# Kernel tuning notes

Hardware: AMD Instinct MI355X
Metric: run time of the kernel (lower is better)

Reference implementation:

```python
import jax, jax.numpy as jnp
import numpy as np

B, CIN, CCTX, K, V, T, KS = 8, 512, 512, 64, 256, 1024, 23
EPS = 1e-5


def _bn(z, gamma, beta):
    # train-mode BatchNorm1d over (batch, time) per channel, biased variance
    mean = jnp.mean(z, axis=(0, 2), keepdims=True)
    var = jnp.mean((z - mean) ** 2, axis=(0, 2), keepdims=True)
    return (z - mean) * jax.lax.rsqrt(var + EPS) * gamma[None, :, None] + beta[None, :, None]


def setup_inputs() -> dict:
    key = jax.random.key(0)
    ks = jax.random.split(key, 10)
    x = jax.random.normal(ks[0], (B, CIN, T), dtype=jnp.float32)
    context = jax.random.normal(ks[1], (B, CCTX, T), dtype=jnp.float32)
    Wq = jax.random.normal(ks[2], (K, CIN), dtype=jnp.float32) * (CIN ** -0.5)
    bq = jnp.zeros((K,), dtype=jnp.float32)
    Wk = jax.random.normal(ks[3], (K, CCTX), dtype=jnp.float32) * (CCTX ** -0.5)
    bk = jnp.zeros((K,), dtype=jnp.float32)
    Wv = jax.random.normal(ks[4], (V, CCTX), dtype=jnp.float32) * (CCTX ** -0.5)
    bv = jnp.zeros((V,), dtype=jnp.float32)
    gamma_q = jnp.ones((K,), dtype=jnp.float32)
    beta_q = jnp.zeros((K,), dtype=jnp.float32)
    gamma_v = jnp.ones((V,), dtype=jnp.float32)
    beta_v = jnp.zeros((V,), dtype=jnp.float32)
    pos_w = jax.random.normal(ks[5], (K, KS), dtype=jnp.float32) * (KS ** -0.5)
    pos_b = jnp.zeros((K,), dtype=jnp.float32)
    return {"x": x, "context": context, "Wq": Wq, "bq": bq, "Wk": Wk, "bk": bk,
            "Wv": Wv, "bv": bv, "gamma_q": gamma_q, "beta_q": beta_q,
            "gamma_v": gamma_v, "beta_v": beta_v, "pos_w": pos_w, "pos_b": pos_b}


def reference(x, context, Wq, bq, Wk, bk, Wv, bv,
              gamma_q, beta_q, gamma_v, beta_v, pos_w, pos_b):
    # 1x1 conv1d == channel matmul
    queries = jnp.einsum('bct,kc->bkt', x, Wq) + bq[None, :, None]          # (B,K,T)
    keys = jnp.einsum('bct,kc->bkt', context, Wk) + bk[None, :, None]       # (B,K,T)
    values = jnp.einsum('bct,vc->bvt', context, Wv) + bv[None, :, None]     # (B,V,T)

    norm_keys = jax.nn.softmax(keys, axis=-1)                               # softmax over T
    queries = _bn(queries, gamma_q, beta_q)
    values = _bn(values, gamma_v, beta_v)

    q_t = jnp.transpose(queries, (0, 2, 1))                                 # (B,T,K)
    v_t = jnp.transpose(values, (0, 2, 1))                                  # (B,T,V)

    content_lambda = jnp.einsum('bkt,btv->bkv', norm_keys, v_t)             # (B,K,V)

    # positional conv2d: kernel (K,1,KS,1), padding (KS//2, 0) along T
    lhs = v_t[:, None, :, :]                                                # (B,1,T,V)
    rhs = pos_w[:, None, :, None]                                           # (K,1,KS,1)
    pl = jax.lax.conv_general_dilated(
        lhs, rhs, window_strides=(1, 1),
        padding=[(KS // 2, KS // 2), (0, 0)],
        dimension_numbers=('NCHW', 'OIHW', 'NCHW'))
    pl = pl + pos_b[None, :, None, None]                                    # (B,K,T,V)
    pl = jnp.transpose(pl, (0, 2, 1, 3))                                    # (B,T,K,V)

    content_out = jnp.einsum('btk,bkv->btv', q_t, content_lambda)           # (B,T,V)
    positional_out = jnp.einsum('btk,btkv->btv', q_t, pl)                   # (B,T,V)

    return jnp.transpose(content_out + positional_out, (0, 2, 1))           # (B,V,T)
```

## Files before the change

kernel.cpp:

```cpp
#include <hip/hip_runtime.h>
#include <math.h>

#define B_ 8
#define CIN_ 512
#define K_ 64
#define V_ 256
#define T_ 1024
#define KS_ 23
#define EPS_ 1e-5f
#define NTC_ 8

typedef __attribute__((ext_vector_type(8))) short bf16x8;
typedef __attribute__((ext_vector_type(4))) float f32x4;

__device__ __forceinline__ unsigned short f2bf(float f) {
    union { float f; unsigned u; } x; x.f = f;
    unsigned r = x.u + 0x7fffu + ((x.u >> 16) & 1u);
    return (unsigned short)(r >> 16);
}
__device__ __forceinline__ float bf2f(unsigned short h) {
    union { unsigned u; float f; } x; x.u = ((unsigned)h) << 16;
    return x.f;
}

__device__ __forceinline__ void gload16(const unsigned short* g, unsigned short* l) {
    __builtin_amdgcn_global_load_lds(
        (const __attribute__((address_space(1))) unsigned int*)(const void*)g,
        (__attribute__((address_space(3))) unsigned int*)(void*)l, 16, 0, 0);
}

__global__ __launch_bounds__(256) void prep_kernel(
    const float* __restrict__ x, const float* __restrict__ ctx,
    const float* __restrict__ Wq, const float* __restrict__ Wk,
    const float* __restrict__ Wv,
    unsigned short* __restrict__ xT, unsigned short* __restrict__ cT,
    unsigned short* __restrict__ Wb, float* __restrict__ stat)
{
    __shared__ unsigned short sh[64][72];
    const int tid = threadIdx.x;
    const int id = blockIdx.x;
    if (id < 2048) {
        const int t0 = (id & 15) * 64, c0 = ((id >> 4) & 7) * 64;
        const int z = id >> 7, b = z & 7, which = z >> 3;
        const float* src = which ? ctx : x;
        unsigned short* dst = which ? cT : xT;
        const int cl = tid >> 2, qq = tid & 3;
        const float* row = src + ((size_t)b * CIN_ + c0 + cl) * T_ + t0 + qq * 16;
        #pragma unroll
        for (int u = 0; u < 4; u++) {
            float4 f = *(const float4*)(row + 4 * u);
            sh[qq * 16 + 4 * u + 0][cl] = f2bf(f.x);
            sh[qq * 16 + 4 * u + 1][cl] = f2bf(f.y);
            sh[qq * 16 + 4 * u + 2][cl] = f2bf(f.z);
            sh[qq * 16 + 4 * u + 3][cl] = f2bf(f.w);
        }
        __syncthreads();
        const int tl = tid >> 2;
        unsigned short* orow = dst + ((size_t)b * T_ + t0 + tl) * CIN_ + c0 + qq * 16;
        *(bf16x8*)(orow)     = *(bf16x8*)&sh[tl][qq * 16];
        *(bf16x8*)(orow + 8) = *(bf16x8*)&sh[tl][qq * 16 + 8];
    } else {
        const int wid = id - 2048;
        if (wid == 0) {
            #pragma unroll
            for (int i = 0; i < 3; i++) {
                int idx = tid + i * 256;
                if (idx < 672) ((float4*)stat)[idx] = make_float4(0.f, 0.f, 0.f, 0.f);
            }
        }
        const int i4 = wid * 256 + tid;
        const int n1 = K_ * CIN_ / 4, n2 = 2 * K_ * CIN_ / 4;
        const float* src; int off;
        if (i4 < n1)      { src = Wq; off = i4; }
        else if (i4 < n2) { src = Wk; off = i4 - n1; }
        else              { src = Wv; off = i4 - n2; }
        float4 f = ((const float4*)src)[off];
        ushort4 h;
        h.x = f2bf(f.x); h.y = f2bf(f.y); h.z = f2bf(f.z); h.w = f2bf(f.w);
        *(ushort4*)(Wb + (size_t)i4 * 4) = h;
    }
}

__global__ __launch_bounds__(256) void proj_mfma5(
    const unsigned short* __restrict__ xT, const unsigned short* __restrict__ cT,
    const unsigned short* __restrict__ Wb,
    const float* __restrict__ bq, const float* __restrict__ bk,
    const float* __restrict__ bv,
    float* __restrict__ k_buf, float* __restrict__ v_raw,
    unsigned short* __restrict__ qT, float* __restrict__ stat,
    float* __restrict__ kml)
{
    __shared__ __align__(16) unsigned short SM[64 * 64 + 128 * 64];
    unsigned short* Wt = SM;
    unsigned short* Xt = SM + 64 * 64;

    const int tid = threadIdx.x;
    const int b = blockIdx.z, t0 = blockIdx.x * 128, yb = blockIdx.y;

    const unsigned short* in; const unsigned short* W; const float* bias;
    float* outp = nullptr; int ch0 = 0; float* ssum = nullptr; float* ssq = nullptr;
    if (yb == 0)      { in = xT; W = Wb;             bias = bq;
                        ssum = stat; ssq = stat + 64; ch0 = 0; }
    else if (yb == 1) { in = cT; W = Wb + K_ * CIN_; bias = bk;
                        outp = k_buf + (size_t)b * K_ * T_; }
    else { int m0 = (yb - 2) * 64; in = cT;
           W = Wb + 2 * K_ * CIN_ + (size_t)m0 * CIN_; bias = bv + m0;
           outp = v_raw + ((size_t)b * V_ + m0) * T_;
           ssum = stat + 128; ssq = stat + 384; ch0 = m0; }

    const int lane = tid & 63, w = tid >> 6;
    const int col = lane & 15, quad = lane >> 4;

    const int gW0 = (0 * 4 + w) * 64 + lane, rW0 = gW0 >> 3;
    const int gW1 = (1 * 4 + w) * 64 + lane, rW1 = gW1 >> 3;
    const unsigned short* sW0 = W + (size_t)rW0 * CIN_ + (((gW0 & 7) ^ (rW0 & 7)) * 8);
    const unsigned short* sW1 = W + (size_t)rW1 * CIN_ + (((gW1 & 7) ^ (rW1 & 7)) * 8);
    unsigned short* dW0 = Wt + (0 * 4 + w) * 512;
    unsigned short* dW1 = Wt + (1 * 4 + w) * 512;

    const int gX0 = (0 * 4 + w) * 64 + lane, rX0 = gX0 >> 3;
    const int gX1 = (1 * 4 + w) * 64 + lane, rX1 = gX1 >> 3;
    const int gX2 = (2 * 4 + w) * 64 + lane, rX2 = gX2 >> 3;
    const int gX3 = (3 * 4 + w) * 64 + lane, rX3 = gX3 >> 3;
    const size_t xbase = (size_t)b * T_ + t0;
    const unsigned short* sX0 = in + (xbase + rX0) * CIN_ + (((gX0 & 7) ^ (rX0 & 7)) * 8);
    const unsigned short* sX1 = in + (xbase + rX1) * CIN_ + (((gX1 & 7) ^ (rX1 & 7)) * 8);
    const unsigned short* sX2 = in + (xbase + rX2) * CIN_ + (((gX2 & 7) ^ (rX2 & 7)) * 8);
    const unsigned short* sX3 = in + (xbase + rX3) * CIN_ + (((gX3 & 7) ^ (rX3 & 7)) * 8);
    unsigned short* dX0 = Xt + (0 * 4 + w) * 512;
    unsigned short* dX1 = Xt + (1 * 4 + w) * 512;
    unsigned short* dX2 = Xt + (2 * 4 + w) * 512;
    unsigned short* dX3 = Xt + (3 * 4 + w) * 512;

    f32x4 acc[8];
    #pragma unroll
    for (int j = 0; j < 8; j++) acc[j] = (f32x4){0.f, 0.f, 0.f, 0.f};

    for (int c0 = 0; c0 < CIN_; c0 += 64) {
        gload16(sW0 + c0, dW0);
        gload16(sW1 + c0, dW1);
        gload16(sX0 + c0, dX0);
        gload16(sX1 + c0, dX1);
        gload16(sX2 + c0, dX2);
        gload16(sX3 + c0, dX3);
        __syncthreads();
        #pragma unroll
        for (int ks = 0; ks < 2; ks++) {
            const int kc = ((ks * 4 + quad) ^ (col & 7)) * 8;
            bf16x8 af = *(bf16x8*)&Wt[(w * 16 + col) * 64 + kc];
            #pragma unroll
            for (int j = 0; j < 8; j++) {
                bf16x8 bfr = *(bf16x8*)&Xt[(j * 16 + col) * 64 + kc];
                acc[j] = __builtin_amdgcn_mfma_f32_16x16x32_bf16(af, bfr, acc[j], 0, 0, 0);
            }
        }
        __syncthreads();
    }

    float bias_v[4], s[4], sq[4], mr[4], lr[4];
    #pragma unroll
    for (int r = 0; r < 4; r++) {
        bias_v[r] = bias[w * 16 + quad * 4 + r];
        s[r] = 0.f; sq[r] = 0.f; mr[r] = -1e30f; lr[r] = 0.f;
    }
    #pragma unroll
    for (int j = 0; j < 8; j++) {
        float o[4];
        #pragma unroll
        for (int r = 0; r < 4; r++) {
            o[r] = acc[j][r] + bias_v[r];
            s[r] += o[r]; sq[r] += o[r] * o[r];
        }
        if (yb == 0) {
            ushort4 h;
            h.x = f2bf(o[0]); h.y = f2bf(o[1]); h.z = f2bf(o[2]); h.w = f2bf(o[3]);
            *(ushort4*)&SM[(j * 16 + col) * 72 + w * 16 + quad * 4] = h;
        } else {
            #pragma unroll
            for (int r = 0; r < 4; r++)
                outp[(size_t)(w * 16 + quad * 4 + r) * T_ + t0 + j * 16 + col] = o[r];
            if (yb == 1) {
                #pragma unroll
                for (int r = 0; r < 4; r++) {
                    float mn = fmaxf(mr[r], o[r]);
                    lr[r] = lr[r] * __expf(mr[r] - mn) + __expf(o[r] - mn);
                    mr[r] = mn;
                }
            }
        }
    }
    if (yb == 0) {
        __syncthreads();
        const int tr = tid >> 1, h2 = tid & 1;
        unsigned short* dq = qT + ((size_t)b * T_ + t0 + tr) * K_ + h2 * 32;
        #pragma unroll
        for (int u = 0; u < 4; u++)
            *(bf16x8*)(dq + u * 8) = *(bf16x8*)&SM[tr * 72 + h2 * 32 + u * 8];
    }
    if (yb == 1) {
        #pragma unroll
        for (int r = 0; r < 4; r++) {
            float m = mr[r], l = lr[r];
            #pragma unroll
            for (int off = 1; off < 16; off <<= 1) {
                float mo = __shfl_xor(m, off, 64);
                float lo = __shfl_xor(l, off, 64);
                float mn = fmaxf(m, mo);
                l = l * __expf(m - mn) + lo * __expf(mo - mn);
                m = mn;
            }
            if (col == 0) {
                int row = w * 16 + quad * 4 + r;
                float* p = kml + (((size_t)b * K_ + row) * 8 + (t0 >> 7)) * 2;
                p[0] = m; p[1] = l;
            }
        }
    } else {
        #pragma unroll
        for (int r = 0; r < 4; r++) {
            float sv = s[r], qv = sq[r];
            #pragma unroll
            for (int off = 1; off < 16; off <<= 1) {
                sv += __shfl_xor(sv, off, 64);
                qv += __shfl_xor(qv, off, 64);
            }
            if (col == 0) {
                int ch = ch0 + w * 16 + quad * 4 + r;
                atomicAdd(&ssum[ch], sv);
                atomicAdd(&ssq[ch], qv);
            }
        }
    }
}

__global__ __launch_bounds__(256) void lambda_kernel5(
    const float* __restrict__ k_buf, const float* __restrict__ v_raw,
    const float* __restrict__ kml, float* __restrict__ clp)
{
    __shared__ __align__(16) float nks[K_][68];
    __shared__ __align__(16) float vls[64][68];
    __shared__ float mrow[64], lrow[64];
    const int tid = threadIdx.x;
    const int b = blockIdx.z, v0 = blockIdx.y * 64, tc = blockIdx.x;

    if (tid < 64) {
        const float2* p = (const float2*)(kml + ((size_t)b * K_ + tid) * 16);
        float m = -1e30f, l = 0.f;
        #pragma unroll
        for (int sgi = 0; sgi < 8; sgi++) {
            float2 ml = p[sgi];
            float mn = fmaxf(m, ml.x);
            l = l * __expf(m - mn) + ml.y * __expf(ml.x - mn);
            m = mn;
        }
        mrow[tid] = m; lrow[tid] = 1.f / l;
    }
    __syncthreads();

    const int r = tid >> 2, q = tid & 3;
    const int tv = tid & 15, tk = tid >> 4;
    float4 acc[4];
    #pragma unroll
    for (int i = 0; i < 4; i++) acc[i] = make_float4(0.f, 0.f, 0.f, 0.f);

    for (int c2 = 0; c2 < 2; c2++) {
        const int t0 = (tc * 2 + c2) * 64;
        if (c2) __syncthreads();
        {
            const float* nrow = k_buf + ((size_t)b * K_ + r) * T_ + t0;
            const float* vrow = v_raw + ((size_t)b * V_ + v0 + r) * T_ + t0;
            const float mr = mrow[r], li = lrow[r];
            #pragma unroll
            for (int i = 0; i < 4; i++) {
                int c4 = q + 4 * i;
                float4 g = *(const float4*)(nrow + 4 * c4);
                g.x = __expf(g.x - mr) * li; g.y = __expf(g.y - mr) * li;
                g.z = __expf(g.z - mr) * li; g.w = __expf(g.w - mr) * li;
                *(float4*)&nks[r][4 * c4] = g;
                float4 h = *(const float4*)(vrow + 4 * c4);
                vls[4 * c4 + 0][r] = h.x; vls[4 * c4 + 1][r] = h.y;
                vls[4 * c4 + 2][r] = h.z; vls[4 * c4 + 3][r] = h.w;
            }
        }
        __syncthreads();
        for (int tt = 0; tt < 16; tt++) {
            float4 w0 = *(float4*)&vls[4 * tt + 0][4 * tv];
            float4 w1 = *(float4*)&vls[4 * tt + 1][4 * tv];
            float4 w2 = *(float4*)&vls[4 * tt + 2][4 * tv];
            float4 w3 = *(float4*)&vls[4 * tt + 3][4 * tv];
            #pragma unroll
            for (int i = 0; i < 4; i++) {
                float4 n = *(float4*)&nks[4 * tk + i][4 * tt];
                acc[i] += w0 * n.x + w1 * n.y + w2 * n.z + w3 * n.w;
            }
        }
    }
    #pragma unroll
    for (int i = 0; i < 4; i++)
        *(float4*)&clp[(((size_t)b * NTC_ + tc) * K_ + 4 * tk + i) * V_ + v0 + 4 * tv] = acc[i];
}

__global__ __launch_bounds__(256) void prep_cl_kernel3(
    const float* __restrict__ clp, const float* __restrict__ stat,
    const float* __restrict__ gq, const float* __restrict__ betaq,
    const float* __restrict__ gv, const float* __restrict__ betav,
    unsigned short* __restrict__ clb2, float* __restrict__ hterm)
{
    __shared__ float qsc[64], qsh[64], red[4][64];
    const int tid = threadIdx.x;
    const int b = blockIdx.y, v0 = blockIdx.x * 64, kz = blockIdx.z;
    const float inv_n = 1.f / (B_ * T_);
    if (tid < 64) {
        float mean = stat[tid] * inv_n;
        float var  = stat[64 + tid] * inv_n - mean * mean;
        float sc = gq[tid] * rsqrtf(var + EPS_);
        qsc[tid] = sc; qsh[tid] = betaq[tid] - mean * sc;
    }
    const int vl = tid & 63, kq = tid >> 6;
    const int c = v0 + vl;
    float vmean = stat[128 + c] * inv_n;
    float vvar  = stat[384 + c] * inv_n - vmean * vmean;
    float vsv = gv[c] * rsqrtf(vvar + EPS_);
    float vhv = betav[c] - vmean * vsv;
    __syncthreads();
    float h = 0.f;
    #pragma unroll
    for (int kk = 0; kk < 4; kk++) {
        int k = kz * 16 + kq * 4 + kk;
        float a = 0.f;
        #pragma unroll
        for (int tc = 0; tc < NTC_; tc++)
            a += clp[(((size_t)b * NTC_ + tc) * K_ + k) * V_ + c];
        float clbv = a * vsv + vhv;
        h += qsh[k] * clbv;
        clb2[((size_t)b * V_ + c) * K_ + k] = f2bf(clbv * qsc[k]);
    }
    red[kq][vl] = h;
    __syncthreads();
    if (tid < 64)
        atomicAdd(&hterm[(size_t)b * V_ + v0 + tid],
                  red[0][tid] + red[1][tid] + red[2][tid] + red[3][tid]);
}

__global__ __launch_bounds__(256) void out_kernel4(
    const unsigned short* __restrict__ qT, const unsigned short* __restrict__ clb2,
    const float* __restrict__ hterm, const float* __restrict__ v_raw,
    const float* __restrict__ stat,
    const float* __restrict__ gq, const float* __restrict__ betaq,
    const float* __restrict__ gv, const float* __restrict__ betav,
    const float* __restrict__ pos_w, const float* __restrict__ pos_b,
    float* __restrict__ out)
{
    __shared__ unsigned short qTt[64][72];
    __shared__ unsigned short clv[64][72];
    __shared__ float vs2T[88][68];
    __shared__ float qpt[64][24];
    __shared__ float pws[64][24];
    __shared__ float qsc[64], qsh[64];
    __shared__ float consts[24];
    __shared__ float hvs[64];
    const int tid = threadIdx.x;
    const int b = blockIdx.z, v0 = blockIdx.y * 64, t0 = blockIdx.x * 64;
    const float inv_n = 1.f / (B_ * T_);

    if (tid < 64) {
        float mean = stat[tid] * inv_n;
        float var  = stat[64 + tid] * inv_n - mean * mean;
        float sc = gq[tid] * rsqrtf(var + EPS_);
        qsc[tid] = sc; qsh[tid] = betaq[tid] - mean * sc;
        hvs[tid] = hterm[(size_t)b * V_ + v0 + tid];
    }
    {
        const int rl = tid >> 2, part = tid & 3;
        const unsigned short* qs = qT + ((size_t)b * T_ + t0 + rl) * K_ + part * 16;
        *(bf16x8*)&qTt[rl][part * 16]     = *(const bf16x8*)(qs);
        *(bf16x8*)&qTt[rl][part * 16 + 8] = *(const bf16x8*)(qs + 8);
        const unsigned short* cs = clb2 + ((size_t)b * V_ + v0 + rl) * K_ + part * 16;
        *(bf16x8*)&clv[rl][part * 16]     = *(const bf16x8*)(cs);
        *(bf16x8*)&clv[rl][part * 16 + 8] = *(const bf16x8*)(cs + 8);
    }
    {
        const int vl = tid >> 2, qq = tid & 3;
        const int c = v0 + vl;
        float vmean = stat[128 + c] * inv_n;
        float vvar  = stat[384 + c] * inv_n - vmean * vmean;
        float vsv = gv[c] * rsqrtf(vvar + EPS_);
        float vhv = betav[c] - vmean * vsv;
        const float* vrow = v_raw + ((size_t)b * V_ + c) * T_;
        #pragma unroll
        for (int i = 0; i < 22; i++) {
            int cc = qq + 4 * i;
            if (cc < 86) {
                int t = t0 + cc - 11;
                vs2T[cc][vl] = (t >= 0 && t < T_) ? vrow[t] * vsv + vhv : 0.f;
            }
        }
    }
    __syncthreads();

    for (int idx = tid; idx < K_ * 24; idx += 256) {
        int k = idx / 24, s = idx % 24;
        pws[k][s] = qsc[k] * (s < KS_ ? pos_w[k * KS_ + s] : pos_b[k]);
    }
    if (tid < 24) {
        float cs = 0.f;
        for (int k = 0; k < K_; k++)
            cs += qsh[k] * (tid < KS_ ? pos_w[k * KS_ + tid] : pos_b[k]);
        consts[tid] = cs;
    }
    __syncthreads();

    {
        const int t = tid >> 2, sg = tid & 3, s0 = sg * 6;
        float a[6];
        #pragma unroll
        for (int u = 0; u < 6; u++) a[u] = consts[s0 + u];
        #pragma unroll
        for (int kb = 0; kb < 8; kb++) {
            bf16x8 qv = *(bf16x8*)&qTt[t][kb * 8];
            #pragma unroll
            for (int j = 0; j < 8; j++) {
                float q = bf2f((unsigned short)qv[j]);
                #pragma unroll
                for (int u = 0; u < 6; u++) a[u] += q * pws[kb * 8 + j][s0 + u];
            }
        }
        #pragma unroll
        for (int u = 0; u < 6; u++) qpt[t][s0 + u] = a[u];
    }
    __syncthreads();

    const int lane = tid & 63, w = tid >> 6;
    const int col = lane & 15, quad = lane >> 4;

    f32x4 acc[4];
    #pragma unroll
    for (int tf = 0; tf < 4; tf++) acc[tf] = (f32x4){0.f, 0.f, 0.f, 0.f};

    #pragma unroll
    for (int ks = 0; ks < 2; ks++) {
        const int kc = ks * 32 + quad * 8;
        bf16x8 af = *(bf16x8*)&clv[w * 16 + col][kc];
        #pragma unroll
        for (int tf = 0; tf < 4; tf++) {
            bf16x8 bq = *(bf16x8*)&qTt[tf * 16 + col][kc];
            acc[tf] = __builtin_amdgcn_mfma_f32_16x16x32_bf16(af, bq, acc[tf], 0, 0, 0);
        }
    }

    const int vb = w * 16 + quad * 4;
    float4 hv4 = *(float4*)&hvs[vb];
    #pragma unroll
    for (int tf = 0; tf < 4; tf++) {
        const int lt = tf * 16 + col;
        float qv[24];
        #pragma unroll
        for (int u = 0; u < 6; u++)
            *(float4*)&qv[4 * u] = *(float4*)&qpt[lt][4 * u];
        float4 a; a.x = acc[tf][0]; a.y = acc[tf][1]; a.z = acc[tf][2]; a.w = acc[tf][3];
        #pragma unroll
        for (int s = 0; s < KS_; s++) {
            float4 wv = *(float4*)&vs2T[lt + s][vb];
            a.x += qv[s] * wv.x; a.y += qv[s] * wv.y;
            a.z += qv[s] * wv.z; a.w += qv[s] * wv.w;
        }
        float base = qv[23];
        a.x += base + hv4.x; a.y += base + hv4.y;
        a.z += base + hv4.z; a.w += base + hv4.w;
        float* ap = (float*)&a;
        #pragma unroll
        for (int r = 0; r < 4; r++)
            out[((size_t)b * V_ + v0 + vb + r) * T_ + t0 + lt] = ap[r];
    }
}

extern "C" void kernel_launch(void* const* d_in, const int* in_sizes, int n_in,
                              void* d_out, int out_size, void* d_ws, size_t ws_size,
                              hipStream_t stream)
{
    const float* x     = (const float*)d_in[0];
    const float* ctx   = (const float*)d_in[1];
    const float* Wq    = (const float*)d_in[2];
    const float* bq    = (const float*)d_in[3];
    const float* Wk    = (const float*)d_in[4];
    const float* bk    = (const float*)d_in[5];
    const float* Wv    = (const float*)d_in[6];
    const float* bv    = (const float*)d_in[7];
    const float* gq    = (const float*)d_in[8];
    const float* betaq = (const float*)d_in[9];
    const float* gv    = (const float*)d_in[10];
    const float* betav = (const float*)d_in[11];
    const float* pos_w = (const float*)d_in[12];
    const float* pos_b = (const float*)d_in[13];
    float* out = (float*)d_out;

    float* ws    = (float*)d_ws;
    float* k_buf = ws;
    float* v_raw = k_buf + (size_t)B_ * K_ * T_;
    float* clp   = v_raw + (size_t)B_ * V_ * T_;
    float* stat  = clp + (size_t)B_ * NTC_ * K_ * V_;
    float* hterm = stat + 640;
    float* kml   = hterm + (size_t)B_ * V_;
    unsigned short* xT   = (unsigned short*)(kml + (size_t)B_ * K_ * 16);
    unsigned short* cT   = xT + (size_t)B_ * T_ * CIN_;
    unsigned short* Wb   = cT + (size_t)B_ * T_ * CIN_;
    unsigned short* qT   = Wb + (size_t)(2 * K_ + V_) * CIN_;
    unsigned short* clb2 = qT + (size_t)B_ * T_ * K_;

    prep_kernel<<<dim3(2048 + 192), 256, 0, stream>>>(
        x, ctx, Wq, Wk, Wv, xT, cT, Wb, stat);
    proj_mfma5<<<dim3(T_ / 128, 6, B_), 256, 0, stream>>>(
        xT, cT, Wb, bq, bk, bv, k_buf, v_raw, qT, stat, kml);
    lambda_kernel5<<<dim3(NTC_, V_ / 64, B_), 256, 0, stream>>>(k_buf, v_raw, kml, clp);
    prep_cl_kernel3<<<dim3(V_ / 64, B_, 4), 256, 0, stream>>>(
        clp, stat, gq, betaq, gv, betav, clb2, hterm);
    out_kernel4<<<dim3(T_ / 64, V_ / 64, B_), 256, 0, stream>>>(
        qT, clb2, hterm, v_raw, stat, gq, betaq, gv, betav, pos_w, pos_b, out);
}
```

Baseline: 150.3 us.

## Double-buffer projection GEMM LDS tiles and pad positional shared array

After: 148.0 us. Within noise of the previous version (-1.5%).

```diff
diff --git a/kernel.cpp b/kernel.cpp
--- a/kernel.cpp
+++ b/kernel.cpp
@@ -81,7 +81,7 @@
     }
 }
 
-__global__ __launch_bounds__(256) void proj_mfma5(
+__global__ __launch_bounds__(256) void proj_mfma6(
     const unsigned short* __restrict__ xT, const unsigned short* __restrict__ cT,
     const unsigned short* __restrict__ Wb,
     const float* __restrict__ bq, const float* __restrict__ bk,
@@ -90,9 +90,7 @@
     unsigned short* __restrict__ qT, float* __restrict__ stat,
     float* __restrict__ kml)
 {
-    __shared__ __align__(16) unsigned short SM[64 * 64 + 128 * 64];
-    unsigned short* Wt = SM;
-    unsigned short* Xt = SM + 64 * 64;
+    __shared__ __align__(16) unsigned short SMb[2][12288];
 
     const int tid = threadIdx.x;
     const int b = blockIdx.z, t0 = blockIdx.x * 128, yb = blockIdx.y;
@@ -115,8 +113,6 @@
     const int gW1 = (1 * 4 + w) * 64 + lane, rW1 = gW1 >> 3;
     const unsigned short* sW0 = W + (size_t)rW0 * CIN_ + (((gW0 & 7) ^ (rW0 & 7)) * 8);
     const unsigned short* sW1 = W + (size_t)rW1 * CIN_ + (((gW1 & 7) ^ (rW1 & 7)) * 8);
-    unsigned short* dW0 = Wt + (0 * 4 + w) * 512;
-    unsigned short* dW1 = Wt + (1 * 4 + w) * 512;
 
     const int gX0 = (0 * 4 + w) * 64 + lane, rX0 = gX0 >> 3;
     const int gX1 = (1 * 4 + w) * 64 + lane, rX1 = gX1 >> 3;
@@ -127,54 +123,71 @@
     const unsigned short* sX1 = in + (xbase + rX1) * CIN_ + (((gX1 & 7) ^ (rX1 & 7)) * 8);
     const unsigned short* sX2 = in + (xbase + rX2) * CIN_ + (((gX2 & 7) ^ (rX2 & 7)) * 8);
     const unsigned short* sX3 = in + (xbase + rX3) * CIN_ + (((gX3 & 7) ^ (rX3 & 7)) * 8);
-    unsigned short* dX0 = Xt + (0 * 4 + w) * 512;
-    unsigned short* dX1 = Xt + (1 * 4 + w) * 512;
-    unsigned short* dX2 = Xt + (2 * 4 + w) * 512;
-    unsigned short* dX3 = Xt + (3 * 4 + w) * 512;
+
+#define STAGE(P, C0) do { \
+    unsigned short* Wt_ = SMb[P]; \
+    unsigned short* Xt_ = SMb[P] + 4096; \
+    gload16(sW0 + (C0), Wt_ + w * 512); \
+    gload16(sW1 + (C0), Wt_ + 2048 + w * 512); \
+    gload16(sX0 + (C0), Xt_ + w * 512); \
+    gload16(sX1 + (C0), Xt_ + 2048 + w * 512); \
+    gload16(sX2 + (C0), Xt_ + 4096 + w * 512); \
+    gload16(sX3 + (C0), Xt_ + 6144 + w * 512); \
+} while (0)
 
     f32x4 acc[8];
     #pragma unroll
     for (int j = 0; j < 8; j++) acc[j] = (f32x4){0.f, 0.f, 0.f, 0.f};
 
-    for (int c0 = 0; c0 < CIN_; c0 += 64) {
-        gload16(sW0 + c0, dW0);
-        gload16(sW1 + c0, dW1);
-        gload16(sX0 + c0, dX0);
-        gload16(sX1 + c0, dX1);
-        gload16(sX2 + c0, dX2);
-        gload16(sX3 + c0, dX3);
-        __syncthreads();
-        #pragma unroll
-        for (int ks = 0; ks < 2; ks++) {
-            const int kc = ((ks * 4 + quad) ^ (col & 7)) * 8;
-            bf16x8 af = *(bf16x8*)&Wt[(w * 16 + col) * 64 + kc];
-            #pragma unroll
-            for (int j = 0; j < 8; j++) {
-                bf16x8 bfr = *(bf16x8*)&Xt[(j * 16 + col) * 64 + kc];
-                acc[j] = __builtin_amdgcn_mfma_f32_16x16x32_bf16(af, bfr, acc[j], 0, 0, 0);
-            }
-        }
-        __syncthreads();
-    }
-
-    float bias_v[4], s[4], sq[4], mr[4], lr[4];
+    STAGE(0, 0);
+    for (int s = 0; s < 8; s++) {
+        const int cur = s & 1;
+        if (s < 7) {
+            STAGE(cur ^ 1, (s + 1) * 64);
+            asm volatile("s_waitcnt vmcnt(6)" ::: "memory");
+        } else {
+            asm volatile("s_waitcnt vmcnt(0)" ::: "memory");
+        }
+        __builtin_amdgcn_s_barrier();
+        __builtin_amdgcn_sched_barrier(0);
+        {
+            const unsigned short* Wt = SMb[cur];
+            const unsigned short* Xt = SMb[cur] + 4096;
+            #pragma unroll
+            for (int ks = 0; ks < 2; ks++) {
+                const int kc = ((ks * 4 + quad) ^ (col & 7)) * 8;
+                bf16x8 af = *(bf16x8*)&Wt[(w * 16 + col) * 64 + kc];
+                #pragma unroll
+                for (int j = 0; j < 8; j++) {
+                    bf16x8 bfr = *(bf16x8*)&Xt[(j * 16 + col) * 64 + kc];
+                    acc[j] = __builtin_amdgcn_mfma_f32_16x16x32_bf16(af, bfr, acc[j], 0, 0, 0);
+                }
+            }
+        }
+        __builtin_amdgcn_sched_barrier(0);
+        __builtin_amdgcn_s_barrier();
+    }
+#undef STAGE
+
+    float bias_v[4], s_[4], sq[4], mr[4], lr[4];
     #pragma unroll
     for (int r = 0; r < 4; r++) {
         bias_v[r] = bias[w * 16 + quad * 4 + r];
-        s[r] = 0.f; sq[r] = 0.f; mr[r] = -1e30f; lr[r] = 0.f;
-    }
+        s_[r] = 0.f; sq[r] = 0.f; mr[r] = -1e30f; lr[r] = 0.f;
+    }
+    unsigned short* SE = SMb[0];
     #pragma unroll
     for (int j = 0; j < 8; j++) {
         float o[4];
         #pragma unroll
         for (int r = 0; r < 4; r++) {
             o[r] = acc[j][r] + bias_v[r];
-            s[r] += o[r]; sq[r] += o[r] * o[r];
+            s_[r] += o[r]; sq[r] += o[r] * o[r];
         }
         if (yb == 0) {
             ushort4 h;
             h.x = f2bf(o[0]); h.y = f2bf(o[1]); h.z = f2bf(o[2]); h.w = f2bf(o[3]);
-            *(ushort4*)&SM[(j * 16 + col) * 72 + w * 16 + quad * 4] = h;
+            *(ushort4*)&SE[(j * 16 + col) * 72 + w * 16 + quad * 4] = h;
         } else {
             #pragma unroll
             for (int r = 0; r < 4; r++)
@@ -195,7 +208,7 @@
         unsigned short* dq = qT + ((size_t)b * T_ + t0 + tr) * K_ + h2 * 32;
         #pragma unroll
         for (int u = 0; u < 4; u++)
-            *(bf16x8*)(dq + u * 8) = *(bf16x8*)&SM[tr * 72 + h2 * 32 + u * 8];
+            *(bf16x8*)(dq + u * 8) = *(bf16x8*)&SE[tr * 72 + h2 * 32 + u * 8];
     }
     if (yb == 1) {
         #pragma unroll
@@ -218,7 +231,7 @@
     } else {
         #pragma unroll
         for (int r = 0; r < 4; r++) {
-            float sv = s[r], qv = sq[r];
+            float sv = s_[r], qv = sq[r];
             #pragma unroll
             for (int off = 1; off < 16; off <<= 1) {
                 sv += __shfl_xor(sv, off, 64);
@@ -342,7 +355,7 @@
                   red[0][tid] + red[1][tid] + red[2][tid] + red[3][tid]);
 }
 
-__global__ __launch_bounds__(256) void out_kernel4(
+__global__ __launch_bounds__(256) void out_kernel5(
     const unsigned short* __restrict__ qT, const unsigned short* __restrict__ clb2,
     const float* __restrict__ hterm, const float* __restrict__ v_raw,
     const float* __restrict__ stat,
@@ -354,7 +367,7 @@
     __shared__ unsigned short qTt[64][72];
     __shared__ unsigned short clv[64][72];
     __shared__ float vs2T[88][68];
-    __shared__ float qpt[64][24];
+    __shared__ float qpt[64][28];
     __shared__ float pws[64][24];
     __shared__ float qsc[64], qsh[64];
     __shared__ float consts[24];
@@ -509,11 +522,11 @@
 
     prep_kernel<<<dim3(2048 + 192), 256, 0, stream>>>(
         x, ctx, Wq, Wk, Wv, xT, cT, Wb, stat);
-    proj_mfma5<<<dim3(T_ / 128, 6, B_), 256, 0, stream>>>(
+    proj_mfma6<<<dim3(T_ / 128, 6, B_), 256, 0, stream>>>(
         xT, cT, Wb, bq, bk, bv, k_buf, v_raw, qT, stat, kml);
     lambda_kernel5<<<dim3(NTC_, V_ / 64, B_), 256, 0, stream>>>(k_buf, v_raw, kml, clp);
     prep_cl_kernel3<<<dim3(V_ / 64, B_, 4), 256, 0, stream>>>(
         clp, stat, gq, betaq, gv, betav, clb2, hterm);
-    out_kernel4<<<dim3(T_ / 64, V_ / 64, B_), 256, 0, stream>>>(
+    out_kernel5<<<dim3(T_ / 64, V_ / 64, B_), 256, 0, stream>>>(
         qT, clb2, hterm, v_raw, stat, gq, betaq, gv, betav, pos_w, pos_b, out);
 }
```
